# Performance work log

Measured on AMD Instinct MI355X. Metric: run time of the kernel, lower is better.

## Reference

```python
import jax, jax.numpy as jnp
import numpy as np

STALENESS_LAMBDA = 0.001
TEMPERATURE = 1.0
TOP_K = 3
EPS = 1e-8


def setup_inputs() -> dict:
    key = jax.random.key(0)
    ks = jax.random.split(key, 6)
    B, D, H, E = 131072, 512, 256, 10
    features = jax.random.normal(ks[0], (B, D), dtype=jnp.float32)
    W_proj = jax.random.normal(ks[1], (D, H), dtype=jnp.float32) * 0.02
    b_proj = jnp.zeros((H,), dtype=jnp.float32)
    expert_emb = jax.random.normal(ks[2], (E, H), dtype=jnp.float32) * 0.01
    expert_features = jax.random.normal(ks[3], (E, D), dtype=jnp.float32)
    trust = jax.random.uniform(ks[4], (E,), dtype=jnp.float32)
    delta_t = jax.random.uniform(ks[5], (E,), dtype=jnp.float32) * 100.0
    return {"features": features, "W_proj": W_proj, "b_proj": b_proj,
            "expert_emb": expert_emb, "expert_features": expert_features,
            "trust": trust, "delta_t": delta_t}


def reference(features, W_proj, b_proj, expert_emb, expert_features, trust, delta_t):
    H = W_proj.shape[1]
    # learned gate: sigmoid(proj(x) . e_j / sqrt(H))  -> (B, E)
    proj = features @ W_proj + b_proj                                  # (B, H)
    gate = jax.nn.sigmoid(jnp.einsum('bh,eh->be', proj, expert_emb)
                          / jnp.sqrt(jnp.float32(H)))
    # cosine similarity S_ij mapped to [0, 1]                          # (B, E)
    fn = features / jnp.maximum(jnp.linalg.norm(features, axis=1, keepdims=True), EPS)
    en = expert_features / jnp.maximum(
        jnp.linalg.norm(expert_features, axis=1, keepdims=True), EPS)
    sim = (jnp.einsum('bd,ed->be', fn, en) + 1.0) * 0.5
    # staleness decay e^{-lambda * dt} and base score T*S*decay
    stale = jnp.exp(-STALENESS_LAMBDA * delta_t)                        # (E,)
    score = gate * (trust * stale)[None, :] * sim                       # (B, E)
    probs = jax.nn.softmax(score / TEMPERATURE, axis=-1)                # (B, E)
    topk_w, topk_idx = jax.lax.top_k(probs, TOP_K)                      # (B, K)
    topk_w = topk_w / jnp.sum(topk_w, axis=-1, keepdims=True)
    return topk_w, topk_idx, probs
```

## Files before the change

### kernel.cpp

```cpp
#include <hip/hip_runtime.h>
#include <stdint.h>
#include <math.h>

#define D_DIM 512
#define H_DIM 256
#define E_NUM 10

typedef float f16v __attribute__((ext_vector_type(16)));
typedef float f2 __attribute__((ext_vector_type(2)));

__global__ __launch_bounds__(256) void pre_wg(const float* __restrict__ Wp,
                                              const float* __restrict__ bp,
                                              const float* __restrict__ emb,
                                              float* __restrict__ pk,
                                              float* __restrict__ bg) {
  int gid = blockIdx.x * 256 + threadIdx.x;
  if (gid < E_NUM * D_DIM) {
    int d = gid / E_NUM;
    int e = gid - d * E_NUM;
    const float* wr = Wp + (size_t)d * H_DIM;
    const float* er = emb + (size_t)e * H_DIM;
    float s0 = 0.f, s1 = 0.f, s2 = 0.f, s3 = 0.f;
#pragma unroll 4
    for (int h = 0; h < H_DIM; h += 4) {
      float4 a = *(const float4*)(wr + h);
      float4 b = *(const float4*)(er + h);
      s0 = fmaf(a.x, b.x, s0); s1 = fmaf(a.y, b.y, s1);
      s2 = fmaf(a.z, b.z, s2); s3 = fmaf(a.w, b.w, s3);
    }
    pk[(size_t)d * 20 + e] = ((s0 + s1) + (s2 + s3)) * 0.0625f;
  } else if (gid < E_NUM * D_DIM + E_NUM) {
    int e = gid - E_NUM * D_DIM;
    const float* er = emb + (size_t)e * H_DIM;
    float s = 0.f;
    for (int h = 0; h < H_DIM; ++h) s = fmaf(bp[h], er[h], s);
    bg[e] = s * 0.0625f;
  }
}

__global__ __launch_bounds__(64) void pre_en(const float* __restrict__ ef,
                                             const float* __restrict__ trust,
                                             const float* __restrict__ dtv,
                                             float* __restrict__ pk,
                                             float* __restrict__ cf) {
  int e = blockIdx.x, l = threadIdx.x;
  const float* row = ef + (size_t)e * D_DIM;
  float s = 0.f;
#pragma unroll
  for (int j = 0; j < D_DIM / 64; ++j) { float v = row[l + 64 * j]; s = fmaf(v, v, s); }
#pragma unroll
  for (int o = 32; o; o >>= 1) s += __shfl_xor(s, o, 64);
  float inv = 1.f / fmaxf(sqrtf(s), 1e-8f);
#pragma unroll
  for (int j = 0; j < D_DIM / 64; ++j) {
    int d = l + 64 * j;
    pk[(size_t)d * 20 + 10 + e] = row[d] * inv;
  }
  if (l == 0) cf[e] = trust[e] * expf(-0.001f * dtv[e]);
}

#define WVx(i) ((i) < 16 ? w0[(i) & 15] : (i) < 32 ? w1[(i) & 15] : \
                (i) < 48 ? w2[(i) & 15] : (i) < 64 ? w3[(i) & 15] : w4[(i) & 15])

__global__ __launch_bounds__(256, 6) void router_main(
    const float* __restrict__ feat, const float* __restrict__ pk,
    const float* __restrict__ cf, const float* __restrict__ bg,
    float* __restrict__ out, int B) {
  __shared__ float lds[6144];
  const int t = threadIdx.x;
  const int l = t & 63;
  const int w = __builtin_amdgcn_readfirstlane(t >> 6);
  const size_t r0 = (size_t)blockIdx.x * 64;

  const float* gsrc = feat + (r0 + w * 16 + (l >> 3)) * (size_t)D_DIM
                      + (((l & 7) ^ (l >> 3)) << 2);
  const int dst0 = w * 512 + (l << 2);

  f2 ag[5], as_[5], n2;
#pragma unroll
  for (int i = 0; i < 5; ++i) { ag[i] = f2{0.f, 0.f}; as_[i] = f2{0.f, 0.f}; }
  n2 = f2{0.f, 0.f};

  auto STAGE = [&](int buf, int c) {
#pragma unroll
    for (int j = 0; j < 2; ++j) {
      __builtin_amdgcn_global_load_lds(
          (const __attribute__((address_space(1))) uint32_t*)(gsrc + (size_t)j * 8 * D_DIM + c * 32),
          (__attribute__((address_space(3))) uint32_t*)&lds[buf * 2048 + dst0 + j * 256],
          16, 0, 0);
    }
  };

  auto COMPUTE = [&](int buf, int c) {
#pragma unroll
    for (int sub = 0; sub < 2; ++sub) {
      f16v w0, w1, w2, w3, w4;
      const float* wp = pk + (size_t)(c * 32 + w * 8 + sub * 4) * 20;
      asm volatile(
          "s_load_dwordx16 %0, %5, 0x0\n"
          "s_load_dwordx16 %1, %5, 0x40\n"
          "s_load_dwordx16 %2, %5, 0x80\n"
          "s_load_dwordx16 %3, %5, 0xc0\n"
          "s_load_dwordx16 %4, %5, 0x100\n"
          "s_waitcnt lgkmcnt(0)"
          : "=&s"(w0), "=&s"(w1), "=&s"(w2), "=&s"(w3), "=&s"(w4)
          : "s"(wp));
      const int slot = (2 * w + sub) ^ (l & 7);
      float4 f = *(const float4*)&lds[buf * 2048 + l * 32 + slot * 4];
#pragma unroll
      for (int q = 0; q < 4; ++q) {
        const float fq = (q == 0) ? f.x : (q == 1) ? f.y : (q == 2) ? f.z : f.w;
        const f2 fq2 = {fq, fq};
#pragma unroll
        for (int j = 0; j < 5; ++j) {
          const int bgi = q * 20 + 2 * j;
          f2 wg2 = {WVx(bgi), WVx(bgi + 1)};
          ag[j] = __builtin_elementwise_fma(fq2, wg2, ag[j]);
        }
#pragma unroll
        for (int j = 0; j < 5; ++j) {
          const int bsi = q * 20 + 10 + 2 * j;
          f2 ws2 = {WVx(bsi), WVx(bsi + 1)};
          as_[j] = __builtin_elementwise_fma(fq2, ws2, as_[j]);
        }
      }
      f2 p0 = {f.x, f.y}, p1 = {f.z, f.w};
      n2 = __builtin_elementwise_fma(p0, p0, n2);
      n2 = __builtin_elementwise_fma(p1, p1, n2);
    }
  };

  STAGE(0, 0); STAGE(1, 1);
  int cb = 0, sb = 2;
#pragma unroll 1
  for (int c = 0; c < 16; ++c) {
    if (c < 15) asm volatile("s_waitcnt vmcnt(2)" ::: "memory");
    else        asm volatile("s_waitcnt vmcnt(0)" ::: "memory");
    __builtin_amdgcn_s_barrier();
    __builtin_amdgcn_sched_barrier(0);
    if (c < 14) STAGE(sb, c + 2);
    COMPUTE(cb, c);
    asm volatile("s_waitcnt lgkmcnt(0)" ::: "memory");
    __builtin_amdgcn_sched_barrier(0);
    cb = (cb == 2) ? 0 : cb + 1;
    sb = (sb == 2) ? 0 : sb + 1;
  }
  __syncthreads();

  float acc[21];
#pragma unroll
  for (int e = 0; e < E_NUM; ++e) { acc[e] = ag[e >> 1][e & 1]; acc[10 + e] = as_[e >> 1][e & 1]; }
  acc[20] = n2.x + n2.y;

  if (w) {
    float* rp = &lds[(w - 1) * 1344 + l * 21];
#pragma unroll
    for (int i = 0; i < 21; ++i) rp[i] = acc[i];
  }
  __syncthreads();
  if (w == 0) {
#pragma unroll
    for (int s = 0; s < 3; ++s) {
      const float* rp = &lds[s * 1344 + l * 21];
#pragma unroll
      for (int i = 0; i < 21; ++i) acc[i] += rp[i];
    }

    const float inv = 1.f / fmaxf(sqrtf(acc[20]), 1e-8f);
    float probs[E_NUM];
    float m = -1e30f;
#pragma unroll
    for (int e = 0; e < E_NUM; ++e) {
      float logit = acc[e] + bg[e];
      float gate = 1.f / (1.f + __expf(-logit));
      float sim = fmaf(acc[10 + e] * inv, 0.5f, 0.5f);
      float sc = gate * cf[e] * sim;
      probs[e] = sc;
      m = fmaxf(m, sc);
    }
    float Z = 0.f;
#pragma unroll
    for (int e = 0; e < E_NUM; ++e) { float pe = __expf(probs[e] - m); probs[e] = pe; Z += pe; }
    const float invZ = 1.f / Z;
#pragma unroll
    for (int e = 0; e < E_NUM; ++e) probs[e] *= invZ;

    int i0 = 0; float b0 = probs[0];
#pragma unroll
    for (int e = 1; e < E_NUM; ++e) if (probs[e] > b0) { b0 = probs[e]; i0 = e; }
    int i1 = -1; float b1 = -1.f;
#pragma unroll
    for (int e = 0; e < E_NUM; ++e) if (e != i0 && probs[e] > b1) { b1 = probs[e]; i1 = e; }
    int i2 = -1; float b2 = -1.f;
#pragma unroll
    for (int e = 0; e < E_NUM; ++e) if (e != i0 && e != i1 && probs[e] > b2) { b2 = probs[e]; i2 = e; }

    const float wnorm = 1.f / (b0 + b1 + b2);
    const size_t row = r0 + l;
    float* ow = out + row * 3;
    ow[0] = b0 * wnorm; ow[1] = b1 * wnorm; ow[2] = b2 * wnorm;
    float* oi = out + (size_t)B * 3 + row * 3;
    oi[0] = (float)i0; oi[1] = (float)i1; oi[2] = (float)i2;
    float* op = out + (size_t)B * 6 + row * E_NUM;
#pragma unroll
    for (int e = 0; e < E_NUM; ++e) op[e] = probs[e];
  }
}

extern "C" void kernel_launch(void* const* d_in, const int* in_sizes, int n_in,
                              void* d_out, int out_size, void* d_ws, size_t ws_size,
                              hipStream_t stream) {
  const float* feat  = (const float*)d_in[0];
  const float* Wp    = (const float*)d_in[1];
  const float* bp    = (const float*)d_in[2];
  const float* emb   = (const float*)d_in[3];
  const float* ef    = (const float*)d_in[4];
  const float* trust = (const float*)d_in[5];
  const float* dtv   = (const float*)d_in[6];
  float* out = (float*)d_out;

  float* pk = (float*)d_ws;
  float* cf = pk + D_DIM * 20;
  float* bg = cf + E_NUM;

  const int B = in_sizes[0] / D_DIM;

  hipLaunchKernelGGL(pre_wg, dim3((E_NUM * D_DIM + E_NUM + 255) / 256), dim3(256),
                     0, stream, Wp, bp, emb, pk, bg);
  hipLaunchKernelGGL(pre_en, dim3(E_NUM), dim3(64), 0, stream, ef, trust, dtv, pk, cf);
  hipLaunchKernelGGL(router_main, dim3(B / 64), dim3(256), 0, stream,
                     feat, pk, cf, bg, out, B);
}
```

Measured before the change: 72.86 us.

## Deepen feature prefetch to four LDS buffers and merge precompute kernels

The main router kernel moves from a three-buffer to a four-buffer LDS ring, keeping three chunk loads in flight instead of two. Buffer indices become c&3, and the vmcnt waits are adjusted to match. LDS per block grows to 32KB and the occupancy hint drops from 6 to 5 blocks. The two small precompute kernels are also fused into one launch, removing one kernel launch and its dependency gap.

```diff
diff --git a/kernel.cpp b/kernel.cpp
--- a/kernel.cpp
+++ b/kernel.cpp
@@ -9,64 +9,69 @@
 typedef float f16v __attribute__((ext_vector_type(16)));
 typedef float f2 __attribute__((ext_vector_type(2)));
 
-__global__ __launch_bounds__(256) void pre_wg(const float* __restrict__ Wp,
-                                              const float* __restrict__ bp,
-                                              const float* __restrict__ emb,
-                                              float* __restrict__ pk,
-                                              float* __restrict__ bg) {
-  int gid = blockIdx.x * 256 + threadIdx.x;
-  if (gid < E_NUM * D_DIM) {
-    int d = gid / E_NUM;
-    int e = gid - d * E_NUM;
-    const float* wr = Wp + (size_t)d * H_DIM;
-    const float* er = emb + (size_t)e * H_DIM;
-    float s0 = 0.f, s1 = 0.f, s2 = 0.f, s3 = 0.f;
+__global__ __launch_bounds__(256) void pre_all(const float* __restrict__ Wp,
+                                               const float* __restrict__ bp,
+                                               const float* __restrict__ emb,
+                                               const float* __restrict__ ef,
+                                               const float* __restrict__ trust,
+                                               const float* __restrict__ dtv,
+                                               float* __restrict__ pk,
+                                               float* __restrict__ bg,
+                                               float* __restrict__ cf) {
+  const int bid = blockIdx.x;
+  if (bid < 20) {
+    int gid = bid * 256 + threadIdx.x;
+    if (gid < E_NUM * D_DIM) {
+      int d = gid / E_NUM;
+      int e = gid - d * E_NUM;
+      const float* wr = Wp + (size_t)d * H_DIM;
+      const float* er = emb + (size_t)e * H_DIM;
+      float s0 = 0.f, s1 = 0.f, s2 = 0.f, s3 = 0.f;
 #pragma unroll 4
-    for (int h = 0; h < H_DIM; h += 4) {
-      float4 a = *(const float4*)(wr + h);
-      float4 b = *(const float4*)(er + h);
-      s0 = fmaf(a.x, b.x, s0); s1 = fmaf(a.y, b.y, s1);
-      s2 = fmaf(a.z, b.z, s2); s3 = fmaf(a.w, b.w, s3);
-    }
-    pk[(size_t)d * 20 + e] = ((s0 + s1) + (s2 + s3)) * 0.0625f;
-  } else if (gid < E_NUM * D_DIM + E_NUM) {
-    int e = gid - E_NUM * D_DIM;
-    const float* er = emb + (size_t)e * H_DIM;
-    float s = 0.f;
-    for (int h = 0; h < H_DIM; ++h) s = fmaf(bp[h], er[h], s);
-    bg[e] = s * 0.0625f;
-  }
-}
-
-__global__ __launch_bounds__(64) void pre_en(const float* __restrict__ ef,
-                                             const float* __restrict__ trust,
-                                             const float* __restrict__ dtv,
-                                             float* __restrict__ pk,
-                                             float* __restrict__ cf) {
-  int e = blockIdx.x, l = threadIdx.x;
-  const float* row = ef + (size_t)e * D_DIM;
-  float s = 0.f;
-#pragma unroll
-  for (int j = 0; j < D_DIM / 64; ++j) { float v = row[l + 64 * j]; s = fmaf(v, v, s); }
-#pragma unroll
-  for (int o = 32; o; o >>= 1) s += __shfl_xor(s, o, 64);
-  float inv = 1.f / fmaxf(sqrtf(s), 1e-8f);
-#pragma unroll
-  for (int j = 0; j < D_DIM / 64; ++j) {
-    int d = l + 64 * j;
-    pk[(size_t)d * 20 + 10 + e] = row[d] * inv;
-  }
-  if (l == 0) cf[e] = trust[e] * expf(-0.001f * dtv[e]);
+      for (int h = 0; h < H_DIM; h += 4) {
+        float4 a = *(const float4*)(wr + h);
+        float4 b = *(const float4*)(er + h);
+        s0 = fmaf(a.x, b.x, s0); s1 = fmaf(a.y, b.y, s1);
+        s2 = fmaf(a.z, b.z, s2); s3 = fmaf(a.w, b.w, s3);
+      }
+      pk[(size_t)d * 20 + e] = ((s0 + s1) + (s2 + s3)) * 0.0625f;
+    }
+  } else {
+    const int t = threadIdx.x;
+    const int l = t & 63;
+    const int w = t >> 6;
+    if (w == 0 && l < E_NUM) {
+      const float* er = emb + (size_t)l * H_DIM;
+      float s = 0.f;
+      for (int h = 0; h < H_DIM; ++h) s = fmaf(bp[h], er[h], s);
+      bg[l] = s * 0.0625f;
+      cf[l] = trust[l] * expf(-0.001f * dtv[l]);
+    }
+    for (int e = w; e < E_NUM; e += 4) {
+      const float* row = ef + (size_t)e * D_DIM;
+      float s = 0.f;
+#pragma unroll
+      for (int j = 0; j < D_DIM / 64; ++j) { float v = row[l + 64 * j]; s = fmaf(v, v, s); }
+#pragma unroll
+      for (int o = 32; o; o >>= 1) s += __shfl_xor(s, o, 64);
+      float inv = 1.f / fmaxf(sqrtf(s), 1e-8f);
+#pragma unroll
+      for (int j = 0; j < D_DIM / 64; ++j) {
+        int d = l + 64 * j;
+        pk[(size_t)d * 20 + 10 + e] = row[d] * inv;
+      }
+    }
+  }
 }
 
 #define WVx(i) ((i) < 16 ? w0[(i) & 15] : (i) < 32 ? w1[(i) & 15] : \
                 (i) < 48 ? w2[(i) & 15] : (i) < 64 ? w3[(i) & 15] : w4[(i) & 15])
 
-__global__ __launch_bounds__(256, 6) void router_main(
+__global__ __launch_bounds__(256, 5) void router_main(
     const float* __restrict__ feat, const float* __restrict__ pk,
     const float* __restrict__ cf, const float* __restrict__ bg,
     float* __restrict__ out, int B) {
-  __shared__ float lds[6144];
+  __shared__ float lds[8192];
   const int t = threadIdx.x;
   const int l = t & 63;
   const int w = __builtin_amdgcn_readfirstlane(t >> 6);
@@ -81,17 +86,18 @@
   for (int i = 0; i < 5; ++i) { ag[i] = f2{0.f, 0.f}; as_[i] = f2{0.f, 0.f}; }
   n2 = f2{0.f, 0.f};
 
-  auto STAGE = [&](int buf, int c) {
+  auto STAGE = [&](int c) {
 #pragma unroll
     for (int j = 0; j < 2; ++j) {
       __builtin_amdgcn_global_load_lds(
           (const __attribute__((address_space(1))) uint32_t*)(gsrc + (size_t)j * 8 * D_DIM + c * 32),
-          (__attribute__((address_space(3))) uint32_t*)&lds[buf * 2048 + dst0 + j * 256],
+          (__attribute__((address_space(3))) uint32_t*)&lds[(c & 3) * 2048 + dst0 + j * 256],
           16, 0, 0);
     }
   };
 
-  auto COMPUTE = [&](int buf, int c) {
+  auto COMPUTE = [&](int c) {
+    const int buf = c & 3;
 #pragma unroll
     for (int sub = 0; sub < 2; ++sub) {
       f16v w0, w1, w2, w3, w4;
@@ -130,20 +136,18 @@
     }
   };
 
-  STAGE(0, 0); STAGE(1, 1);
-  int cb = 0, sb = 2;
+  STAGE(0); STAGE(1); STAGE(2);
 #pragma unroll 1
   for (int c = 0; c < 16; ++c) {
-    if (c < 15) asm volatile("s_waitcnt vmcnt(2)" ::: "memory");
-    else        asm volatile("s_waitcnt vmcnt(0)" ::: "memory");
+    if (c <= 13)      asm volatile("s_waitcnt vmcnt(4)" ::: "memory");
+    else if (c == 14) asm volatile("s_waitcnt vmcnt(2)" ::: "memory");
+    else              asm volatile("s_waitcnt vmcnt(0)" ::: "memory");
     __builtin_amdgcn_s_barrier();
     __builtin_amdgcn_sched_barrier(0);
-    if (c < 14) STAGE(sb, c + 2);
-    COMPUTE(cb, c);
+    if (c < 13) STAGE(c + 3);
+    COMPUTE(c);
     asm volatile("s_waitcnt lgkmcnt(0)" ::: "memory");
     __builtin_amdgcn_sched_barrier(0);
-    cb = (cb == 2) ? 0 : cb + 1;
-    sb = (sb == 2) ? 0 : sb + 1;
   }
   __syncthreads();
 
@@ -225,9 +229,8 @@
 
   const int B = in_sizes[0] / D_DIM;
 
-  hipLaunchKernelGGL(pre_wg, dim3((E_NUM * D_DIM + E_NUM + 255) / 256), dim3(256),
-                     0, stream, Wp, bp, emb, pk, bg);
-  hipLaunchKernelGGL(pre_en, dim3(E_NUM), dim3(64), 0, stream, ef, trust, dtv, pk, cf);
+  hipLaunchKernelGGL(pre_all, dim3(21), dim3(256), 0, stream,
+                     Wp, bp, emb, ef, trust, dtv, pk, bg, cf);
   hipLaunchKernelGGL(router_main, dim3(B / 64), dim3(256), 0, stream,
                      feat, pk, cf, bg, out, B);
 }
```

Result: faster. 69.28 us, median of 2 (-4.9%).
